# Kernel optimization log

Hardware: AMD Instinct MI355X
Metric: run time of the kernel (lower is better)

## Reference

```python
import jax, jax.numpy as jnp
import numpy as np

B, T, HE, L, HD = 512, 512, 512, 64, 512

def setup_inputs() -> dict:
    key = jax.random.key(0)
    ks = jax.random.split(key, 16)
    def w(k, shape):
        return jax.random.normal(k, shape, dtype=jnp.float32) * 0.05
    z32 = lambda n: jnp.zeros((n,), jnp.float32)
    return {
        "input_tensor": jax.random.normal(ks[0], (B, T, 1), dtype=jnp.float32),
        # encoder LSTMCell (keras gate order i, f, g, o)
        "enc_W": w(ks[1], (1, 4 * HE)),
        "enc_U": w(ks[2], (HE, 4 * HE)),
        "enc_b": z32(4 * HE),
        # encoder mu / std heads
        "emu_W": w(ks[3], (HE, L)), "emu_b": z32(L),
        "estd_W": w(ks[4], (HE, L)), "estd_b": z32(L),
        # decoder first-state dense (tanh)
        "dfs_W": w(ks[5], (L, HD)), "dfs_b": z32(HD),
        # decoder LSTMCell
        "dec_W": w(ks[6], (L, 4 * HD)),
        "dec_U": w(ks[7], (HD, 4 * HD)),
        "dec_b": z32(4 * HD),
        # decoder mu / std heads (Dense(1))
        "dmu_W": w(ks[8], (HD, 1)), "dmu_b": z32(1),
        "dstd_W": w(ks[9], (HD, 1)), "dstd_b": z32(1),
    }

def _lstm_update(gates, c):
    i, f, g, o = jnp.split(gates, 4, axis=-1)
    c_new = jax.nn.sigmoid(f) * c + jax.nn.sigmoid(i) * jnp.tanh(g)
    h_new = jax.nn.sigmoid(o) * jnp.tanh(c_new)
    return h_new, c_new

def reference(input_tensor, enc_W, enc_U, enc_b, emu_W, emu_b, estd_W, estd_b,
              dfs_W, dfs_b, dec_W, dec_U, dec_b, dmu_W, dmu_b, dstd_W, dstd_b):
    x = input_tensor
    Bn, Tn = x.shape[0], x.shape[1]
    He = enc_U.shape[0]

    # ---- encoder: LSTM over time, keep final h ----
    def enc_step(carry, xt):
        h, c = carry
        gates = xt @ enc_W + h @ enc_U + enc_b
        return _lstm_update(gates, c), None
    h0 = jnp.zeros((Bn, He), x.dtype)
    (hT, _), _ = jax.lax.scan(enc_step, (h0, h0), jnp.swapaxes(x, 0, 1))

    mu_enc = hT @ emu_W + emu_b                       # [B, L]
    sigma_enc = jax.nn.softplus(hT @ estd_W + estd_b)  # [B, L]
    z = mu_enc  # call() uses reparam=False -> latent returns mu

    # ---- decoder: LSTM fed constant z each step ----
    hd = jnp.tanh(z @ dfs_W + dfs_b)                  # [B, HD]
    cd = jnp.zeros_like(hd)
    zin = z @ dec_W + dec_b                           # input projection constant over t
    def dec_step(carry, _):
        h, c = carry
        h_new, c_new = _lstm_update(zin + h @ dec_U, c)
        mu = h_new @ dmu_W + dmu_b                    # [B, 1]
        sg = h_new @ dstd_W + dstd_b
        return (h_new, c_new), (mu, sg)
    _, (mus, sgs) = jax.lax.scan(dec_step, (hd, cd), None, length=Tn)

    mu_dec = jnp.swapaxes(mus, 0, 1)                  # [B, T, 1]
    sigma_dec = jax.nn.softplus(jnp.swapaxes(sgs, 0, 1))
    return (mu_dec, sigma_dec, mu_enc, sigma_enc)
```

## Files before the change

### kernel.cpp

```cpp
#include <hip/hip_runtime.h>


#define B_ 512
#define T_ 512
#define H_ 512

typedef _Float16 f16;
typedef _Float16 f16x8 __attribute__((ext_vector_type(8)));
typedef float f32x16 __attribute__((ext_vector_type(16)));
typedef unsigned long long u64;
typedef unsigned int u32;

#define OFF_SG_DEC 262144
#define OFF_MU_ENC 524288
#define OFF_SG_ENC 557056

__device__ __forceinline__ float sigm_(float x) { return 1.f / (1.f + __expf(-x)); }
__device__ __forceinline__ float tanh_(float x) {
  float t = fabsf(x);
  float e = __expf(2.f * t);
  float r = 1.f - 2.f / (e + 1.f);
  return x < 0.f ? -r : r;
}
__device__ __forceinline__ float softplus_(float x) {
  return fmaxf(x, 0.f) + log1pf(__expf(-fabsf(x)));
}
__device__ __forceinline__ int fresh_(u64 w, u32 g) {
  return ((u32)(w >> 48) == g) & (((u32)(w >> 16) & 0xffffu) == g);
}
__device__ __forceinline__ u32 packh_(u64 w) {
  return (u32)(w & 0xffffu) | (((u32)(w >> 32) & 0xffffu) << 16);
}

__global__ void pack_U(const float* __restrict__ U, f16* __restrict__ Upk) {
  const int e = blockIdx.x * 256 + threadIdx.x;
  const int j = e & 7, lane = (e >> 3) & 63, ks = (e >> 9) & 31;
  const int w = (e >> 14) & 7, wg = (e >> 17) & 7;
  const int ccol = lane & 31, khalf = lane >> 5;
  const int uu = ccol >> 2, gate = ccol & 3;
  const int k = ks * 16 + khalf * 8 + j;
  const int gcol = gate * 512 + wg * 64 + w * 8 + uu;
  Upk[e] = (f16)U[k * 2048 + gcol];
}

template <int IS_DEC>
__global__ void __launch_bounds__(512, 1)
lstm_rec(const f16* __restrict__ Upk,
         const float* __restrict__ xin,
         const float* __restrict__ wa,
         const float* __restrict__ wb,
         u32* __restrict__ hbuf,
         float* __restrict__ accmu,
         float* __restrict__ accsg) {
  const int bid = blockIdx.x;
  const int s = bid >> 3;
  const int j = (bid & 7) * 4 + (s & 3);
  const int wg = s >> 2;
  const int tid = threadIdx.x, wave = tid >> 6, lane = tid & 63;
  const int U0 = wg * 64;
  const int RA = j * 16, RB = j * 16 + 8;
  const u32 GB = IS_DEC ? 0x8000u : 0u;
  const int ccol = lane & 31, khalf = lane >> 5;

  f16x8 Breg[32];
#pragma unroll
  for (int ks = 0; ks < 32; ++ks) {
    const f16* p = Upk + (((wg * 8 + wave) * 32 + ks) << 9) + lane * 8;
    asm volatile("global_load_dwordx4 %0, %1, off\n\ts_waitcnt vmcnt(0)"
                 : "=v"(Breg[ks]) : "v"(p));
  }

  const int p_ = ccol & 3, uu_ = ccol >> 2;
  const int row_l = p_ + 4 * khalf;
  const int unit_l = wave * 8 + uu_;
  float biasv[4], xwv[4], addA[4], addB[4];
#pragma unroll
  for (int gt = 0; gt < 4; ++gt) {
    const int col = gt * 512 + U0 + unit_l;
    if (IS_DEC) {
      addA[gt] = xin[(RA + row_l) * 2048 + col];
      addB[gt] = xin[(RB + row_l) * 2048 + col];
      biasv[gt] = 0.f; xwv[gt] = 0.f;
    } else {
      biasv[gt] = wb[col];
      xwv[gt] = wa[col];
      addA[gt] = 0.f; addB[gt] = 0.f;
    }
  }
  float wmu[8], wsg[8];
  if (IS_DEC) {
#pragma unroll
    for (int q = 0; q < 8; ++q) {
      wmu[q] = wa[lane * 8 + q];
      wsg[q] = wb[lane * 8 + q];
    }
  }

  float cA = 0.f, cB = 0.f;

  __shared__ __align__(16) f16 bufA[8 * 520];
  __shared__ __align__(16) f16 bufB[8 * 520];

  int lrow[4], lcol[4], gidxA[4], gidxB[4];
#pragma unroll
  for (int i = 0; i < 4; ++i) {
    const int w = tid + i * 512;
    lrow[i] = w >> 8; lcol[i] = w & 255;
    gidxA[i] = (RA + lrow[i]) * 256 + lcol[i];
    gidxB[i] = (RB + lrow[i]) * 256 + lcol[i];
  }
  const u64* hb64 = (const u64*)hbuf;

  u64 wAr[4], wBr[4];
#pragma unroll
  for (int i = 0; i < 4; ++i)
    wAr[i] = __hip_atomic_load(hb64 + gidxA[i], __ATOMIC_RELAXED,
                               __HIP_MEMORY_SCOPE_AGENT);
  asm volatile("" ::: "memory");

  for (int t = 0; t < T_; ++t) {
    const int b0 = (t & 1) * 131072;
    const int b1 = ((t + 1) & 1) * 131072;
    const int c1 = ((t + 1) & 1) * 262144;
    const u32 gr = GB + (u32)t, gn = GB + (u32)t + 1u;
    const int duty = IS_DEC && t >= 1 && wg == (t & 7);

    while (!(fresh_(wAr[0], gr) & fresh_(wAr[1], gr) &
             fresh_(wAr[2], gr) & fresh_(wAr[3], gr))) {
#pragma unroll
      for (int i = 0; i < 4; ++i)
        wAr[i] = __hip_atomic_load(hb64 + b0 + gidxA[i], __ATOMIC_RELAXED,
                                   __HIP_MEMORY_SCOPE_AGENT);
    }
#pragma unroll
    for (int i = 0; i < 4; ++i)
      *(u32*)&bufA[lrow[i] * 520 + lcol[i] * 2] = packh_(wAr[i]);
    __syncthreads();

#pragma unroll
    for (int i = 0; i < 4; ++i)
      wBr[i] = __hip_atomic_load(hb64 + b0 + gidxB[i], __ATOMIC_RELAXED,
                                 __HIP_MEMORY_SCOPE_AGENT);
    asm volatile("" ::: "memory");

    if (duty) {
      const f16x8 hv = *(const f16x8*)&bufA[wave * 520 + lane * 8];
      float smu = 0.f, ssg = 0.f;
#pragma unroll
      for (int q = 0; q < 8; ++q) {
        const float hq = (float)hv[q];
        smu += hq * wmu[q]; ssg += hq * wsg[q];
      }
#pragma unroll
      for (int o = 32; o; o >>= 1) {
        smu += __shfl_xor(smu, o); ssg += __shfl_xor(ssg, o);
      }
      if (lane == 0) {
        accmu[(RA + wave) * 512 + (t - 1)] = smu;
        accsg[(RA + wave) * 512 + (t - 1)] = ssg;
      }
    }

    {
      float xv = 0.f;
      if (!IS_DEC) xv = xin[(RA + row_l) * T_ + t];
      f32x16 acc;
#pragma unroll
      for (int q = 0; q < 16; ++q) acc[q] = 0.f;
#pragma unroll
      for (int ks = 0; ks < 32; ++ks) {
        f16x8 a = *(const f16x8*)&bufA[(lane & 7) * 520 + ks * 16 + khalf * 8];
        acc = __builtin_amdgcn_mfma_f32_32x32x16_f16(a, Breg[ks], acc, 0, 0, 0);
      }
      const float x0 = acc[0], x1 = acc[1], x2 = acc[2], x3 = acc[3];
      const int odd1 = lane & 1, odd2 = lane & 2;
      const float t0 = __shfl_xor(x1, 1), t1 = __shfl_xor(x0, 1);
      const float t2 = __shfl_xor(x3, 1), t3 = __shfl_xor(x2, 1);
      const float y0 = odd1 ? t0 : x0, y1 = odd1 ? x1 : t1;
      const float y2 = odd1 ? t2 : x2, y3 = odd1 ? x3 : t3;
      const float s0 = __shfl_xor(y2, 2), s1 = __shfl_xor(y3, 2);
      const float s2 = __shfl_xor(y0, 2), s3 = __shfl_xor(y1, 2);
      const float z0 = odd2 ? s0 : y0, z1 = odd2 ? s1 : y1;
      const float z2 = odd2 ? y2 : s2, z3 = odd2 ? y3 : s3;
      float ga0, ga1, ga2, ga3;
      if (IS_DEC) {
        ga0 = z0 + addA[0]; ga1 = z1 + addA[1];
        ga2 = z2 + addA[2]; ga3 = z3 + addA[3];
      } else {
        ga0 = z0 + biasv[0] + xv * xwv[0];
        ga1 = z1 + biasv[1] + xv * xwv[1];
        ga2 = z2 + biasv[2] + xv * xwv[2];
        ga3 = z3 + biasv[3] + xv * xwv[3];
      }
      const float cn = sigm_(ga1) * cA + sigm_(ga0) * tanh_(ga2);
      cA = cn;
      const float hn = sigm_(ga3) * tanh_(cn);
      union { f16 h; unsigned short u; } hc; hc.h = (f16)hn;
      __hip_atomic_store(hbuf + c1 + (RA + row_l) * 512 + U0 + unit_l,
                         (gn << 16) | (u32)hc.u, __ATOMIC_RELAXED,
                         __HIP_MEMORY_SCOPE_AGENT);
    }

    while (!(fresh_(wBr[0], gr) & fresh_(wBr[1], gr) &
             fresh_(wBr[2], gr) & fresh_(wBr[3], gr))) {
#pragma unroll
      for (int i = 0; i < 4; ++i)
        wBr[i] = __hip_atomic_load(hb64 + b0 + gidxB[i], __ATOMIC_RELAXED,
                                   __HIP_MEMORY_SCOPE_AGENT);
    }
#pragma unroll
    for (int i = 0; i < 4; ++i)
      *(u32*)&bufB[lrow[i] * 520 + lcol[i] * 2] = packh_(wBr[i]);
    __syncthreads();

#pragma unroll
    for (int i = 0; i < 4; ++i)
      wAr[i] = __hip_atomic_load(hb64 + b1 + gidxA[i], __ATOMIC_RELAXED,
                                 __HIP_MEMORY_SCOPE_AGENT);
    asm volatile("" ::: "memory");

    if (duty) {
      const f16x8 hv = *(const f16x8*)&bufB[wave * 520 + lane * 8];
      float smu = 0.f, ssg = 0.f;
#pragma unroll
      for (int q = 0; q < 8; ++q) {
        const float hq = (float)hv[q];
        smu += hq * wmu[q]; ssg += hq * wsg[q];
      }
#pragma unroll
      for (int o = 32; o; o >>= 1) {
        smu += __shfl_xor(smu, o); ssg += __shfl_xor(ssg, o);
      }
      if (lane == 0) {
        accmu[(RB + wave) * 512 + (t - 1)] = smu;
        accsg[(RB + wave) * 512 + (t - 1)] = ssg;
      }
    }

    {
      float xv = 0.f;
      if (!IS_DEC) xv = xin[(RB + row_l) * T_ + t];
      f32x16 acc;
#pragma unroll
      for (int q = 0; q < 16; ++q) acc[q] = 0.f;
#pragma unroll
      for (int ks = 0; ks < 32; ++ks) {
        f16x8 a = *(const f16x8*)&bufB[(lane & 7) * 520 + ks * 16 + khalf * 8];
        acc = __builtin_amdgcn_mfma_f32_32x32x16_f16(a, Breg[ks], acc, 0, 0, 0);
      }
      const float x0 = acc[0], x1 = acc[1], x2 = acc[2], x3 = acc[3];
      const int odd1 = lane & 1, odd2 = lane & 2;
      const float t0 = __shfl_xor(x1, 1), t1 = __shfl_xor(x0, 1);
      const float t2 = __shfl_xor(x3, 1), t3 = __shfl_xor(x2, 1);
      const float y0 = odd1 ? t0 : x0, y1 = odd1 ? x1 : t1;
      const float y2 = odd1 ? t2 : x2, y3 = odd1 ? x3 : t3;
      const float s0 = __shfl_xor(y2, 2), s1 = __shfl_xor(y3, 2);
      const float s2 = __shfl_xor(y0, 2), s3 = __shfl_xor(y1, 2);
      const float z0 = odd2 ? s0 : y0, z1 = odd2 ? s1 : y1;
      const float z2 = odd2 ? y2 : s2, z3 = odd2 ? y3 : s3;
      float ga0, ga1, ga2, ga3;
      if (IS_DEC) {
        ga0 = z0 + addB[0]; ga1 = z1 + addB[1];
        ga2 = z2 + addB[2]; ga3 = z3 + addB[3];
      } else {
        ga0 = z0 + biasv[0] + xv * xwv[0];
        ga1 = z1 + biasv[1] + xv * xwv[1];
        ga2 = z2 + biasv[2] + xv * xwv[2];
        ga3 = z3 + biasv[3] + xv * xwv[3];
      }
      const float cn = sigm_(ga1) * cB + sigm_(ga0) * tanh_(ga2);
      cB = cn;
      const float hn = sigm_(ga3) * tanh_(cn);
      union { f16 h; unsigned short u; } hc; hc.h = (f16)hn;
      __hip_atomic_store(hbuf + c1 + (RB + row_l) * 512 + U0 + unit_l,
                         (gn << 16) | (u32)hc.u, __ATOMIC_RELAXED,
                         __HIP_MEMORY_SCOPE_AGENT);
    }
  }
}

__global__ void dec_tail(const u32* __restrict__ hbuf, const float* __restrict__ dmuW,
                         const float* __restrict__ dstdW, float* __restrict__ accmu,
                         float* __restrict__ accsg) {
  const int r = blockIdx.x, lane = threadIdx.x;
  float smu = 0.f, ssg = 0.f;
#pragma unroll
  for (int q = 0; q < 8; ++q) {
    union { unsigned short u; f16 h; } c;
    c.u = (unsigned short)(hbuf[r * 512 + lane * 8 + q] & 0xffffu);
    const float hq = (float)c.h;
    smu += hq * dmuW[lane * 8 + q];
    ssg += hq * dstdW[lane * 8 + q];
  }
#pragma unroll
  for (int o = 32; o; o >>= 1) {
    smu += __shfl_xor(smu, o); ssg += __shfl_xor(ssg, o);
  }
  if (lane == 0) {
    accmu[r * 512 + 511] = smu;
    accsg[r * 512 + 511] = ssg;
  }
}

__global__ void enc_heads(const u32* __restrict__ h0, const float* __restrict__ emuW,
                          const float* __restrict__ emub, const float* __restrict__ estdW,
                          const float* __restrict__ estdb, float* __restrict__ out,
                          float* __restrict__ z) {
  const int b = blockIdx.x, tid = threadIdx.x;
  __shared__ float hrow[512];
  for (int k = tid; k < 512; k += 128) {
    union { unsigned short u; f16 h; } c;
    c.u = (unsigned short)(h0[b * 512 + k] & 0xffffu);
    hrow[k] = (float)c.h;
  }
  __syncthreads();
  const int head = tid >> 6, l = tid & 63;
  const float* W = head ? estdW : emuW;
  float a = 0.f;
#pragma unroll 8
  for (int k = 0; k < 512; ++k) a += hrow[k] * W[k * 64 + l];
  if (head == 0) {
    const float v = a + emub[l];
    out[OFF_MU_ENC + b * 64 + l] = v;
    z[b * 64 + l] = v;
  } else {
    out[OFF_SG_ENC + b * 64 + l] = softplus_(a + estdb[l]);
  }
}

__global__ void dec_prep(const float* __restrict__ z, const float* __restrict__ dfsW,
                         const float* __restrict__ dfsb, const float* __restrict__ decW,
                         const float* __restrict__ decb, u32* __restrict__ hbuf,
                         float* __restrict__ zin) {
  const int b = blockIdx.x, tid = threadIdx.x;
  __shared__ float zl[64];
  if (tid < 64) zl[tid] = z[b * 64 + tid];
  __syncthreads();
  for (int c = tid; c < 512; c += 256) {
    float a = dfsb[c];
#pragma unroll
    for (int l = 0; l < 64; ++l) a += zl[l] * dfsW[l * 512 + c];
    union { f16 h; unsigned short u; } hc; hc.h = (f16)tanh_(a);
    hbuf[b * 512 + c] = (0x8000u << 16) | (u32)hc.u;
  }
  for (int c = tid; c < 2048; c += 256) {
    float a = decb[c];
#pragma unroll
    for (int l = 0; l < 64; ++l) a += zl[l] * decW[l * 2048 + c];
    zin[b * 2048 + c] = a;
  }
}

__global__ void finalize_k(const float* __restrict__ accmu, const float* __restrict__ accsg,
                           const float* __restrict__ dmub, const float* __restrict__ dstdb,
                           float* __restrict__ out) {
  const int i = blockIdx.x * 256 + threadIdx.x;
  out[i] = accmu[i] + dmub[0];
  out[OFF_SG_DEC + i] = softplus_(accsg[i] + dstdb[0]);
}

extern "C" void kernel_launch(void* const* d_in, const int* in_sizes, int n_in,
                              void* d_out, int out_size, void* d_ws, size_t ws_size,
                              hipStream_t stream) {
  (void)in_sizes; (void)n_in; (void)out_size; (void)ws_size;
  const float* x     = (const float*)d_in[0];
  const float* encW  = (const float*)d_in[1];
  const float* encU  = (const float*)d_in[2];
  const float* encb  = (const float*)d_in[3];
  const float* emuW  = (const float*)d_in[4];
  const float* emub  = (const float*)d_in[5];
  const float* estdW = (const float*)d_in[6];
  const float* estdb = (const float*)d_in[7];
  const float* dfsW  = (const float*)d_in[8];
  const float* dfsb  = (const float*)d_in[9];
  const float* decW  = (const float*)d_in[10];
  const float* decU  = (const float*)d_in[11];
  const float* decb  = (const float*)d_in[12];
  const float* dmuW  = (const float*)d_in[13];
  const float* dmub  = (const float*)d_in[14];
  const float* dstdW = (const float*)d_in[15];
  const float* dstdb = (const float*)d_in[16];

  char* ws = (char*)d_ws;
  u32*   hbuf  = (u32*)(ws + 0);
  float* accmu = (float*)(ws + (2u << 20));
  float* accsg = (float*)(ws + (3u << 20));
  f16*   UpkE  = (f16*)(ws + (4u << 20));
  float* zin   = (float*)(ws + (4u << 20));
  f16*   UpkD  = (f16*)(ws + (8u << 20));
  float* z     = (float*)(ws + (10u << 20));
  float* out   = (float*)d_out;

  hipMemsetAsync(d_ws, 0, 2u << 20, stream);

  hipLaunchKernelGGL(pack_U, dim3(4096), dim3(256), 0, stream, encU, UpkE);
  hipLaunchKernelGGL(pack_U, dim3(4096), dim3(256), 0, stream, decU, UpkD);

  hipLaunchKernelGGL((lstm_rec<0>), dim3(256), dim3(512), 0, stream,
                     UpkE, x, encW, encb, hbuf, (float*)nullptr, (float*)nullptr);
  hipLaunchKernelGGL(enc_heads, dim3(512), dim3(128), 0, stream,
                     hbuf, emuW, emub, estdW, estdb, out, z);
  hipLaunchKernelGGL(dec_prep, dim3(512), dim3(256), 0, stream,
                     z, dfsW, dfsb, decW, decb, hbuf, zin);
  hipLaunchKernelGGL((lstm_rec<1>), dim3(256), dim3(512), 0, stream,
                     UpkD, zin, dmuW, dstdW, hbuf, accmu, accsg);
  hipLaunchKernelGGL(dec_tail, dim3(512), dim3(64), 0, stream,
                     hbuf, dmuW, dstdW, accmu, accsg);
  hipLaunchKernelGGL(finalize_k, dim3(1024), dim3(256), 0, stream,
                     accmu, accsg, dmub, dstdb, out);
}
```

Before: 5.101 ms.

## Process all 16 batch rows in one 32x32 MFMA per step, stage x in LDS

```diff
diff --git a/kernel.cpp b/kernel.cpp
--- a/kernel.cpp
+++ b/kernel.cpp
@@ -54,11 +54,11 @@
          float* __restrict__ accsg) {
   const int bid = blockIdx.x;
   const int s = bid >> 3;
-  const int j = (bid & 7) * 4 + (s & 3);
+  const int g = (bid & 7) * 4 + (s & 3);
   const int wg = s >> 2;
   const int tid = threadIdx.x, wave = tid >> 6, lane = tid & 63;
   const int U0 = wg * 64;
-  const int RA = j * 16, RB = j * 16 + 8;
+  const int R0 = g * 16;
   const u32 GB = IS_DEC ? 0x8000u : 0u;
   const int ccol = lane & 31, khalf = lane >> 5;
 
@@ -71,20 +71,20 @@
   }
 
   const int p_ = ccol & 3, uu_ = ccol >> 2;
-  const int row_l = p_ + 4 * khalf;
+  const int r_lo = p_ + 4 * khalf, r_hi = r_lo + 8;
   const int unit_l = wave * 8 + uu_;
-  float biasv[4], xwv[4], addA[4], addB[4];
+  float biasv[4], xwv[4], addLo[4], addHi[4];
 #pragma unroll
   for (int gt = 0; gt < 4; ++gt) {
     const int col = gt * 512 + U0 + unit_l;
     if (IS_DEC) {
-      addA[gt] = xin[(RA + row_l) * 2048 + col];
-      addB[gt] = xin[(RB + row_l) * 2048 + col];
+      addLo[gt] = xin[(R0 + r_lo) * 2048 + col];
+      addHi[gt] = xin[(R0 + r_hi) * 2048 + col];
       biasv[gt] = 0.f; xwv[gt] = 0.f;
     } else {
       biasv[gt] = wb[col];
       xwv[gt] = wa[col];
-      addA[gt] = 0.f; addB[gt] = 0.f;
+      addLo[gt] = 0.f; addHi[gt] = 0.f;
     }
   }
   float wmu[8], wsg[8];
@@ -96,185 +96,160 @@
     }
   }
 
-  float cA = 0.f, cB = 0.f;
-
-  __shared__ __align__(16) f16 bufA[8 * 520];
-  __shared__ __align__(16) f16 bufB[8 * 520];
-
-  int lrow[4], lcol[4], gidxA[4], gidxB[4];
-#pragma unroll
-  for (int i = 0; i < 4; ++i) {
+  float cLo = 0.f, cHi = 0.f;
+
+  __shared__ __align__(16) f16 bufs[2][16 * 520];
+  __shared__ float xl[16 * 516];
+
+  if (!IS_DEC) {
+#pragma unroll
+    for (int i = 0; i < 16; ++i) {
+      const int idx = tid + i * 512;
+      const int r = idx >> 9, c2 = idx & 511;
+      xl[r * 516 + c2] = xin[(R0 + r) * T_ + c2];
+    }
+  }
+
+  int srow[8], scol[8], gidx[8];
+#pragma unroll
+  for (int i = 0; i < 8; ++i) {
     const int w = tid + i * 512;
-    lrow[i] = w >> 8; lcol[i] = w & 255;
-    gidxA[i] = (RA + lrow[i]) * 256 + lcol[i];
-    gidxB[i] = (RB + lrow[i]) * 256 + lcol[i];
+    srow[i] = w >> 8; scol[i] = w & 255;
+    gidx[i] = (R0 + srow[i]) * 256 + scol[i];
   }
   const u64* hb64 = (const u64*)hbuf;
 
-  u64 wAr[4], wBr[4];
-#pragma unroll
-  for (int i = 0; i < 4; ++i)
-    wAr[i] = __hip_atomic_load(hb64 + gidxA[i], __ATOMIC_RELAXED,
-                               __HIP_MEMORY_SCOPE_AGENT);
+  u64 wr[8];
+#pragma unroll
+  for (int i = 0; i < 8; ++i)
+    wr[i] = __hip_atomic_load(hb64 + gidx[i], __ATOMIC_RELAXED,
+                              __HIP_MEMORY_SCOPE_AGENT);
   asm volatile("" ::: "memory");
 
   for (int t = 0; t < T_; ++t) {
     const int b0 = (t & 1) * 131072;
     const int b1 = ((t + 1) & 1) * 131072;
     const int c1 = ((t + 1) & 1) * 262144;
-    const u32 gr = GB + (u32)t, gn = GB + (u32)t + 1u;
-    const int duty = IS_DEC && t >= 1 && wg == (t & 7);
-
-    while (!(fresh_(wAr[0], gr) & fresh_(wAr[1], gr) &
-             fresh_(wAr[2], gr) & fresh_(wAr[3], gr))) {
-#pragma unroll
-      for (int i = 0; i < 4; ++i)
-        wAr[i] = __hip_atomic_load(hb64 + b0 + gidxA[i], __ATOMIC_RELAXED,
-                                   __HIP_MEMORY_SCOPE_AGENT);
-    }
-#pragma unroll
-    for (int i = 0; i < 4; ++i)
-      *(u32*)&bufA[lrow[i] * 520 + lcol[i] * 2] = packh_(wAr[i]);
+    const u32 gr = GB + (u32)t, gn = gr + 1u;
+
+    for (;;) {
+      int f = 1;
+#pragma unroll
+      for (int i = 0; i < 8; ++i) f &= fresh_(wr[i], gr);
+      if (f) break;
+#pragma unroll
+      for (int i = 0; i < 8; ++i)
+        wr[i] = __hip_atomic_load(hb64 + b0 + gidx[i], __ATOMIC_RELAXED,
+                                  __HIP_MEMORY_SCOPE_AGENT);
+    }
+    f16* const sb = bufs[t & 1];
+#pragma unroll
+    for (int i = 0; i < 8; ++i)
+      *(u32*)&sb[srow[i] * 520 + scol[i] * 2] = packh_(wr[i]);
     __syncthreads();
 
-#pragma unroll
-    for (int i = 0; i < 4; ++i)
-      wBr[i] = __hip_atomic_load(hb64 + b0 + gidxB[i], __ATOMIC_RELAXED,
-                                 __HIP_MEMORY_SCOPE_AGENT);
-    asm volatile("" ::: "memory");
-
-    if (duty) {
-      const f16x8 hv = *(const f16x8*)&bufA[wave * 520 + lane * 8];
-      float smu = 0.f, ssg = 0.f;
-#pragma unroll
-      for (int q = 0; q < 8; ++q) {
-        const float hq = (float)hv[q];
-        smu += hq * wmu[q]; ssg += hq * wsg[q];
-      }
-#pragma unroll
-      for (int o = 32; o; o >>= 1) {
-        smu += __shfl_xor(smu, o); ssg += __shfl_xor(ssg, o);
-      }
-      if (lane == 0) {
-        accmu[(RA + wave) * 512 + (t - 1)] = smu;
-        accsg[(RA + wave) * 512 + (t - 1)] = ssg;
-      }
-    }
-
-    {
-      float xv = 0.f;
-      if (!IS_DEC) xv = xin[(RA + row_l) * T_ + t];
-      f32x16 acc;
-#pragma unroll
-      for (int q = 0; q < 16; ++q) acc[q] = 0.f;
-#pragma unroll
-      for (int ks = 0; ks < 32; ++ks) {
-        f16x8 a = *(const f16x8*)&bufA[(lane & 7) * 520 + ks * 16 + khalf * 8];
-        acc = __builtin_amdgcn_mfma_f32_32x32x16_f16(a, Breg[ks], acc, 0, 0, 0);
-      }
+    f32x16 acc;
+#pragma unroll
+    for (int q = 0; q < 16; ++q) acc[q] = 0.f;
+#pragma unroll
+    for (int ks = 0; ks < 32; ++ks) {
+      f16x8 a = *(const f16x8*)&sb[(lane & 15) * 520 + ks * 16 + khalf * 8];
+      acc = __builtin_amdgcn_mfma_f32_32x32x16_f16(a, Breg[ks], acc, 0, 0, 0);
+    }
+
+    const int odd1 = lane & 1, odd2 = lane & 2;
+    float gLo0, gLo1, gLo2, gLo3, gHi0, gHi1, gHi2, gHi3;
+    {
       const float x0 = acc[0], x1 = acc[1], x2 = acc[2], x3 = acc[3];
-      const int odd1 = lane & 1, odd2 = lane & 2;
       const float t0 = __shfl_xor(x1, 1), t1 = __shfl_xor(x0, 1);
       const float t2 = __shfl_xor(x3, 1), t3 = __shfl_xor(x2, 1);
       const float y0 = odd1 ? t0 : x0, y1 = odd1 ? x1 : t1;
       const float y2 = odd1 ? t2 : x2, y3 = odd1 ? x3 : t3;
       const float s0 = __shfl_xor(y2, 2), s1 = __shfl_xor(y3, 2);
       const float s2 = __shfl_xor(y0, 2), s3 = __shfl_xor(y1, 2);
-      const float z0 = odd2 ? s0 : y0, z1 = odd2 ? s1 : y1;
-      const float z2 = odd2 ? y2 : s2, z3 = odd2 ? y3 : s3;
-      float ga0, ga1, ga2, ga3;
-      if (IS_DEC) {
-        ga0 = z0 + addA[0]; ga1 = z1 + addA[1];
-        ga2 = z2 + addA[2]; ga3 = z3 + addA[3];
-      } else {
-        ga0 = z0 + biasv[0] + xv * xwv[0];
-        ga1 = z1 + biasv[1] + xv * xwv[1];
-        ga2 = z2 + biasv[2] + xv * xwv[2];
-        ga3 = z3 + biasv[3] + xv * xwv[3];
-      }
-      const float cn = sigm_(ga1) * cA + sigm_(ga0) * tanh_(ga2);
-      cA = cn;
-      const float hn = sigm_(ga3) * tanh_(cn);
-      union { f16 h; unsigned short u; } hc; hc.h = (f16)hn;
-      __hip_atomic_store(hbuf + c1 + (RA + row_l) * 512 + U0 + unit_l,
-                         (gn << 16) | (u32)hc.u, __ATOMIC_RELAXED,
-                         __HIP_MEMORY_SCOPE_AGENT);
-    }
-
-    while (!(fresh_(wBr[0], gr) & fresh_(wBr[1], gr) &
-             fresh_(wBr[2], gr) & fresh_(wBr[3], gr))) {
-#pragma unroll
-      for (int i = 0; i < 4; ++i)
-        wBr[i] = __hip_atomic_load(hb64 + b0 + gidxB[i], __ATOMIC_RELAXED,
-                                   __HIP_MEMORY_SCOPE_AGENT);
-    }
-#pragma unroll
-    for (int i = 0; i < 4; ++i)
-      *(u32*)&bufB[lrow[i] * 520 + lcol[i] * 2] = packh_(wBr[i]);
-    __syncthreads();
-
-#pragma unroll
-    for (int i = 0; i < 4; ++i)
-      wAr[i] = __hip_atomic_load(hb64 + b1 + gidxA[i], __ATOMIC_RELAXED,
-                                 __HIP_MEMORY_SCOPE_AGENT);
-    asm volatile("" ::: "memory");
-
-    if (duty) {
-      const f16x8 hv = *(const f16x8*)&bufB[wave * 520 + lane * 8];
-      float smu = 0.f, ssg = 0.f;
-#pragma unroll
-      for (int q = 0; q < 8; ++q) {
-        const float hq = (float)hv[q];
-        smu += hq * wmu[q]; ssg += hq * wsg[q];
-      }
-#pragma unroll
-      for (int o = 32; o; o >>= 1) {
-        smu += __shfl_xor(smu, o); ssg += __shfl_xor(ssg, o);
-      }
-      if (lane == 0) {
-        accmu[(RB + wave) * 512 + (t - 1)] = smu;
-        accsg[(RB + wave) * 512 + (t - 1)] = ssg;
-      }
-    }
-
-    {
-      float xv = 0.f;
-      if (!IS_DEC) xv = xin[(RB + row_l) * T_ + t];
-      f32x16 acc;
-#pragma unroll
-      for (int q = 0; q < 16; ++q) acc[q] = 0.f;
-#pragma unroll
-      for (int ks = 0; ks < 32; ++ks) {
-        f16x8 a = *(const f16x8*)&bufB[(lane & 7) * 520 + ks * 16 + khalf * 8];
-        acc = __builtin_amdgcn_mfma_f32_32x32x16_f16(a, Breg[ks], acc, 0, 0, 0);
-      }
-      const float x0 = acc[0], x1 = acc[1], x2 = acc[2], x3 = acc[3];
-      const int odd1 = lane & 1, odd2 = lane & 2;
+      gLo0 = odd2 ? s0 : y0; gLo1 = odd2 ? s1 : y1;
+      gLo2 = odd2 ? y2 : s2; gLo3 = odd2 ? y3 : s3;
+    }
+    {
+      const float x0 = acc[4], x1 = acc[5], x2 = acc[6], x3 = acc[7];
       const float t0 = __shfl_xor(x1, 1), t1 = __shfl_xor(x0, 1);
       const float t2 = __shfl_xor(x3, 1), t3 = __shfl_xor(x2, 1);
       const float y0 = odd1 ? t0 : x0, y1 = odd1 ? x1 : t1;
       const float y2 = odd1 ? t2 : x2, y3 = odd1 ? x3 : t3;
       const float s0 = __shfl_xor(y2, 2), s1 = __shfl_xor(y3, 2);
       const float s2 = __shfl_xor(y0, 2), s3 = __shfl_xor(y1, 2);
-      const float z0 = odd2 ? s0 : y0, z1 = odd2 ? s1 : y1;
-      const float z2 = odd2 ? y2 : s2, z3 = odd2 ? y3 : s3;
+      gHi0 = odd2 ? s0 : y0; gHi1 = odd2 ? s1 : y1;
+      gHi2 = odd2 ? y2 : s2; gHi3 = odd2 ? y3 : s3;
+    }
+
+    float hnLo, hnHi;
+    {
       float ga0, ga1, ga2, ga3;
       if (IS_DEC) {
-        ga0 = z0 + addB[0]; ga1 = z1 + addB[1];
-        ga2 = z2 + addB[2]; ga3 = z3 + addB[3];
+        ga0 = gLo0 + addLo[0]; ga1 = gLo1 + addLo[1];
+        ga2 = gLo2 + addLo[2]; ga3 = gLo3 + addLo[3];
       } else {
-        ga0 = z0 + biasv[0] + xv * xwv[0];
-        ga1 = z1 + biasv[1] + xv * xwv[1];
-        ga2 = z2 + biasv[2] + xv * xwv[2];
-        ga3 = z3 + biasv[3] + xv * xwv[3];
-      }
-      const float cn = sigm_(ga1) * cB + sigm_(ga0) * tanh_(ga2);
-      cB = cn;
-      const float hn = sigm_(ga3) * tanh_(cn);
-      union { f16 h; unsigned short u; } hc; hc.h = (f16)hn;
-      __hip_atomic_store(hbuf + c1 + (RB + row_l) * 512 + U0 + unit_l,
-                         (gn << 16) | (u32)hc.u, __ATOMIC_RELAXED,
+        const float xv = xl[r_lo * 516 + t];
+        ga0 = gLo0 + biasv[0] + xv * xwv[0];
+        ga1 = gLo1 + biasv[1] + xv * xwv[1];
+        ga2 = gLo2 + biasv[2] + xv * xwv[2];
+        ga3 = gLo3 + biasv[3] + xv * xwv[3];
+      }
+      const float cn = sigm_(ga1) * cLo + sigm_(ga0) * tanh_(ga2);
+      cLo = cn;
+      hnLo = sigm_(ga3) * tanh_(cn);
+    }
+    {
+      float ga0, ga1, ga2, ga3;
+      if (IS_DEC) {
+        ga0 = gHi0 + addHi[0]; ga1 = gHi1 + addHi[1];
+        ga2 = gHi2 + addHi[2]; ga3 = gHi3 + addHi[3];
+      } else {
+        const float xv = xl[r_hi * 516 + t];
+        ga0 = gHi0 + biasv[0] + xv * xwv[0];
+        ga1 = gHi1 + biasv[1] + xv * xwv[1];
+        ga2 = gHi2 + biasv[2] + xv * xwv[2];
+        ga3 = gHi3 + biasv[3] + xv * xwv[3];
+      }
+      const float cn = sigm_(ga1) * cHi + sigm_(ga0) * tanh_(ga2);
+      cHi = cn;
+      hnHi = sigm_(ga3) * tanh_(cn);
+    }
+
+    {
+      union { f16 h; unsigned short u; } a, b;
+      a.h = (f16)hnLo; b.h = (f16)hnHi;
+      __hip_atomic_store(hbuf + c1 + (R0 + r_lo) * 512 + U0 + unit_l,
+                         (gn << 16) | (u32)a.u, __ATOMIC_RELAXED,
                          __HIP_MEMORY_SCOPE_AGENT);
+      __hip_atomic_store(hbuf + c1 + (R0 + r_hi) * 512 + U0 + unit_l,
+                         (gn << 16) | (u32)b.u, __ATOMIC_RELAXED,
+                         __HIP_MEMORY_SCOPE_AGENT);
+    }
+
+#pragma unroll
+    for (int i = 0; i < 8; ++i)
+      wr[i] = __hip_atomic_load(hb64 + b1 + gidx[i], __ATOMIC_RELAXED,
+                                __HIP_MEMORY_SCOPE_AGENT);
+    asm volatile("" ::: "memory");
+
+    if (IS_DEC && t >= 1 && wave < 2) {
+      const int hr = 2 * wg + wave;
+      const f16x8 hv = *(const f16x8*)&sb[hr * 520 + lane * 8];
+      float smu = 0.f, ssg = 0.f;
+#pragma unroll
+      for (int q = 0; q < 8; ++q) {
+        const float hq = (float)hv[q];
+        smu += hq * wmu[q]; ssg += hq * wsg[q];
+      }
+#pragma unroll
+      for (int o = 32; o; o >>= 1) {
+        smu += __shfl_xor(smu, o); ssg += __shfl_xor(ssg, o);
+      }
+      if (lane == 0) {
+        accmu[(R0 + hr) * 512 + (t - 1)] = smu;
+        accsg[(R0 + hr) * 512 + (t - 1)] = ssg;
+      }
     }
   }
 }
```

Result: slower. 9.009 ms (+76.6%).
